# Kernel optimization log

Measured on AMD Instinct MI355X. Metric: run time of the kernel, lower is better.

Reference implementation:

```python
import jax, jax.numpy as jnp
import numpy as np

EMB = 1024
HEADS = 16
HEAD_DIM = EMB // HEADS
MASK_VAL = -10000.0


def setup_inputs() -> dict:
    key = jax.random.key(0)
    ks = jax.random.split(key, 5)
    B, S = 4, 2048
    x = jax.random.normal(ks[0], (B, S, EMB), dtype=jnp.float32)
    scale = 1.0 / np.sqrt(EMB)
    w_qkv = jax.random.normal(ks[1], (EMB, 3 * EMB), dtype=jnp.float32) * scale
    b_qkv = jnp.zeros((3 * EMB,), dtype=jnp.float32)
    w_fc = jax.random.normal(ks[2], (EMB, EMB), dtype=jnp.float32) * scale
    b_fc = jnp.zeros((EMB,), dtype=jnp.float32)
    return {"x": x, "w_qkv": w_qkv, "b_qkv": b_qkv, "w_fc": w_fc, "b_fc": b_fc}


def reference(x, w_qkv, b_qkv, w_fc, b_fc):
    B, S, _ = x.shape
    qkv = x @ w_qkv + b_qkv                      # (B, S, 3*EMB)
    q, k, v = jnp.split(qkv, 3, axis=-1)
    # split heads: (B, S, EMB) -> (B, H, S, Dh)
    def sh(t):
        return t.reshape(B, S, HEADS, HEAD_DIM).transpose(0, 2, 1, 3)
    q, k, v = sh(q), sh(k), sh(v)
    scores = jnp.einsum('bhqd,bhkd->bhqk', q, k) / np.sqrt(HEAD_DIM)
    causal = jnp.tril(jnp.ones((S, S), dtype=bool))[None, None]
    scores = jnp.where(causal, scores, jnp.float32(MASK_VAL))
    probs = jax.nn.softmax(scores, axis=-1)
    out = jnp.einsum('bhqk,bhkd->bhqd', probs, v)
    out = out.transpose(0, 2, 1, 3).reshape(B, S, EMB)  # merge heads
    return out @ w_fc + b_fc
```

## Files before the change

kernel.cpp:

```cpp
#include <hip/hip_runtime.h>
#include <hip/hip_bf16.h>
#include <cstdint>

#define BF16 __hip_bfloat16

typedef __attribute__((ext_vector_type(8))) short bhalf8;
typedef __attribute__((ext_vector_type(4))) float floatx4;

#define MFMA16(a, b, c) __builtin_amdgcn_mfma_f32_16x16x32_bf16((a), (b), (c), 0, 0, 0)

#define MASKV (-30000.0f)
#define QSCALE 0.18033688011112042f

__device__ __forceinline__ void async_cp16(const void* gsrc, void* ldst) {
  __builtin_amdgcn_global_load_lds(
      (__attribute__((address_space(1))) void*)(size_t)gsrc,
      (__attribute__((address_space(3))) void*)ldst, 16, 0, 0);
}

__device__ __forceinline__ bhalf8 cvt8(const float* p) {
  const float4 f0 = *(const float4*)p;
  const float4 f1 = *(const float4*)(p + 4);
  union { bhalf8 v; ushort u[8]; } r;
  const float t[8] = {f0.x, f0.y, f0.z, f0.w, f1.x, f1.y, f1.z, f1.w};
#pragma unroll
  for (int i = 0; i < 8; ++i) {
    BF16 h = __float2bfloat16(t[i]);
    r.u[i] = *(const ushort*)&h;
  }
  return r.v;
}

__global__ void cvt_f32_bf16(const float* __restrict__ in, BF16* __restrict__ out) {
  const size_t i = ((size_t)blockIdx.x * 256 + threadIdx.x) * 8;
  *(bhalf8*)(out + i) = cvt8(in + i);
}

__global__ void transpose_cvt(const float* __restrict__ in, ushort* __restrict__ out,
                              int R, int C) {
  __shared__ ushort t[32][33];
  const int c0 = blockIdx.x * 32, r0 = blockIdx.y * 32;
  const int tx = threadIdx.x, ty = threadIdx.y;
#pragma unroll
  for (int j = 0; j < 32; j += 8) {
    BF16 h = __float2bfloat16(in[(size_t)(r0 + ty + j) * C + c0 + tx]);
    t[ty + j][tx] = *(const ushort*)&h;
  }
  __syncthreads();
#pragma unroll
  for (int j = 0; j < 32; j += 8)
    out[(size_t)(c0 + ty + j) * R + r0 + tx] = t[tx][ty + j];
}

template <int MODE>
__global__ __launch_bounds__(256, 2) void gemm_bt(
    const BF16* __restrict__ A, const BF16* __restrict__ Bt, const float* __restrict__ bias,
    void* __restrict__ C0v, BF16* __restrict__ C1, BF16* __restrict__ C2,
    int Md, int Nd, int Kd) {
  __shared__ __align__(16) BF16 As[128 * 64];
  __shared__ __align__(16) BF16 Bs[128 * 64];

  const int tid = threadIdx.x;
  const int w = tid >> 6, lane = tid & 63;
  const int lm = lane & 15, quad = lane >> 4;
  const int wm = (w >> 1) * 64, wn = (w & 1) * 64;
  const int tile_m = blockIdx.y * 128, tile_n = blockIdx.x * 128;

  floatx4 acc[4][4];
#pragma unroll
  for (int i = 0; i < 4; ++i)
#pragma unroll
    for (int j = 0; j < 4; ++j) acc[i][j] = (floatx4){0.f, 0.f, 0.f, 0.f};

  for (int k0 = 0; k0 < Kd; k0 += 64) {
    __syncthreads();
#pragma unroll
    for (int j = 0; j < 4; ++j) {
      const int sb = (j * 4 + w) * 64;
      const int slot = sb + lane;
      const int row = slot >> 3;
      const int gs = ((slot & 7) - row) & 7;
      async_cp16(A + (size_t)(tile_m + row) * Kd + k0 + gs * 8, As + sb * 8);
      async_cp16(Bt + (size_t)(tile_n + row) * Kd + k0 + gs * 8, Bs + sb * 8);
    }
    __syncthreads();

#pragma unroll
    for (int s = 0; s < 2; ++s) {
      bhalf8 af[4], bfr[4];
#pragma unroll
      for (int mt = 0; mt < 4; ++mt) {
        const int r = wm + mt * 16 + lm;
        const int g = ((s * 4 + quad) + r) & 7;
        af[mt] = *(const bhalf8*)(As + r * 64 + g * 8);
      }
#pragma unroll
      for (int nt = 0; nt < 4; ++nt) {
        const int r = wn + nt * 16 + lm;
        const int g = ((s * 4 + quad) + r) & 7;
        bfr[nt] = *(const bhalf8*)(Bs + r * 64 + g * 8);
      }
#pragma unroll
      for (int mt = 0; mt < 4; ++mt)
#pragma unroll
        for (int nt = 0; nt < 4; ++nt)
          acc[mt][nt] = MFMA16(af[mt], bfr[nt], acc[mt][nt]);
    }
  }

#pragma unroll
  for (int nt = 0; nt < 4; ++nt) {
    const int n = tile_n + wn + nt * 16 + lm;
    const float bv = bias[n];
#pragma unroll
    for (int mt = 0; mt < 4; ++mt) {
      const int m0 = tile_m + wm + mt * 16 + quad * 4;
      floatx4 v = acc[mt][nt];
      if (MODE == 0) {
        float* C0f = (float*)C0v;
#pragma unroll
        for (int r = 0; r < 4; ++r)
          C0f[(size_t)(m0 + r) * Nd + n] = v[r] + bv;
      } else {
        const int which = n >> 10;
        const int h = (n >> 6) & 15;
        const int d = n & 63;
        if (which == 2) {
          const int b = m0 >> 11, s0 = m0 & 2047;
          union { ushort4 u4; ushort u[4]; } pk;
#pragma unroll
          for (int r = 0; r < 4; ++r) {
            BF16 hv = __float2bfloat16(v[r] + bv);
            pk.u[r] = *(const ushort*)&hv;
          }
          *(ushort4*)(C2 + ((size_t)((b * 16 + h) * 64 + d)) * 2048 + s0) = pk.u4;
        } else {
          BF16* dst = (which == 0) ? (BF16*)C0v : C1;
          const float sc = (which == 0) ? QSCALE : 1.0f;
#pragma unroll
          for (int r = 0; r < 4; ++r) {
            const int m = m0 + r, b = m >> 11, si = m & 2047;
            dst[((size_t)(b * 16 + h) * 2048 + si) * 64 + d] =
                __float2bfloat16((v[r] + bv) * sc);
          }
        }
      }
    }
  }
}

__global__ __launch_bounds__(256, 2) void flash_attn(
    const BF16* __restrict__ Q, const BF16* __restrict__ Kmat,
    const BF16* __restrict__ VT, BF16* __restrict__ O) {
  __shared__ __align__(16) BF16 Ks[64 * 64];
  __shared__ __align__(16) BF16 Vs[64 * 64];
  __shared__ __align__(16) BF16 Ps[4 * 32 * 64];

  const int bh = blockIdx.y;
  const int qt = (int)gridDim.x - 1 - (int)blockIdx.x;
  const int tid = threadIdx.x;
  const int w = tid >> 6, lane = tid & 63;
  const int lm = lane & 15, quad = lane >> 4;
  const size_t bh_off = (size_t)bh * (2048 * 64);

  const int qb0 = qt * 128 + w * 32;

  bhalf8 aq[2][2];
#pragma unroll
  for (int s2 = 0; s2 < 2; ++s2) {
    const size_t qoff = bh_off + (size_t)(qb0 + s2 * 16 + lm) * 64;
    aq[s2][0] = *(const bhalf8*)(Q + qoff + quad * 8);
    aq[s2][1] = *(const bhalf8*)(Q + qoff + 32 + quad * 8);
  }

  floatx4 oacc[2][4];
  float m_i[2], l_i[2];
#pragma unroll
  for (int s2 = 0; s2 < 2; ++s2) {
    m_i[s2] = MASKV;
    l_i[s2] = 0.f;
#pragma unroll
    for (int i = 0; i < 4; ++i) oacc[s2][i] = (floatx4){0.f, 0.f, 0.f, 0.f};
  }

  int srow[2], sgs[2], sslot[2];
#pragma unroll
  for (int j = 0; j < 2; ++j) {
    const int slot = (w * 2 + j) * 64 + lane;
    sslot[j] = slot;
    srow[j] = slot >> 3;
    sgs[j] = ((slot & 7) - (slot >> 3)) & 7;
  }
  BF16* pw = Ps + w * (32 * 64);

  bhalf8 kv[2], vv[2], nkv[2], nvv[2];
  {
    const BF16* Kg = Kmat + bh_off;
    const BF16* Vg = VT + bh_off;
#pragma unroll
    for (int j = 0; j < 2; ++j) {
      kv[j] = *(const bhalf8*)(Kg + srow[j] * 64 + sgs[j] * 8);
      vv[j] = *(const bhalf8*)(Vg + (size_t)srow[j] * 2048 + sgs[j] * 8);
    }
  }

  const int ktmax = 2 * qt + 1;
  for (int kt = 0; kt <= ktmax; ++kt) {
    __syncthreads();
#pragma unroll
    for (int j = 0; j < 2; ++j) {
      *(bhalf8*)(Ks + sslot[j] * 8) = kv[j];
      *(bhalf8*)(Vs + sslot[j] * 8) = vv[j];
    }
    __syncthreads();

    if (kt < ktmax) {
      const BF16* Kg = Kmat + bh_off + (size_t)((kt + 1) * 64) * 64;
      const BF16* Vg = VT + bh_off + (kt + 1) * 64;
#pragma unroll
      for (int j = 0; j < 2; ++j) {
        nkv[j] = *(const bhalf8*)(Kg + srow[j] * 64 + sgs[j] * 8);
        nvv[j] = *(const bhalf8*)(Vg + (size_t)srow[j] * 2048 + sgs[j] * 8);
      }
    }

    const int k0 = kt * 64;
#pragma unroll
    for (int s2 = 0; s2 < 2; ++s2) {
      const int qb = qb0 + s2 * 16;
      if (k0 > qb + 15) continue;

      floatx4 st[4];
#pragma unroll
      for (int nt = 0; nt < 4; ++nt) {
        const int rr = nt * 16 + lm;
        const bhalf8 ak0 = *(const bhalf8*)(Ks + rr * 64 + ((quad + rr) & 7) * 8);
        const bhalf8 ak1 = *(const bhalf8*)(Ks + rr * 64 + ((4 + quad + rr) & 7) * 8);
        floatx4 z = (floatx4){0.f, 0.f, 0.f, 0.f};
        z = MFMA16(ak0, aq[s2][0], z);
        z = MFMA16(ak1, aq[s2][1], z);
        st[nt] = z;
      }

      if (k0 + 63 > qb) {
#pragma unroll
        for (int nt = 0; nt < 4; ++nt)
#pragma unroll
          for (int r = 0; r < 4; ++r)
            if ((k0 + nt * 16 + quad * 4 + r) > (qb + lm)) st[nt][r] = MASKV;
      }

      float mx = MASKV;
#pragma unroll
      for (int nt = 0; nt < 4; ++nt)
#pragma unroll
        for (int r = 0; r < 4; ++r) mx = fmaxf(mx, st[nt][r]);
      mx = fmaxf(mx, __shfl_xor(mx, 16, 64));
      mx = fmaxf(mx, __shfl_xor(mx, 32, 64));
      const float mnew = fmaxf(m_i[s2], mx);
      const float alpha = __builtin_amdgcn_exp2f(m_i[s2] - mnew);
      m_i[s2] = mnew;

      float rs = 0.f;
#pragma unroll
      for (int nt = 0; nt < 4; ++nt)
#pragma unroll
        for (int r = 0; r < 4; ++r) {
          const float p = __builtin_amdgcn_exp2f(st[nt][r] - mnew);
          st[nt][r] = p;
          rs += p;
        }
      rs += __shfl_xor(rs, 16, 64);
      rs += __shfl_xor(rs, 32, 64);
      l_i[s2] = l_i[s2] * alpha + rs;
#pragma unroll
      for (int dn = 0; dn < 4; ++dn) oacc[s2][dn] *= alpha;

      BF16* pws = pw + s2 * (16 * 64);
#pragma unroll
      for (int nt = 0; nt < 4; ++nt) {
        union { ushort4 u4; ushort u[4]; } pk;
#pragma unroll
        for (int r = 0; r < 4; ++r) {
          BF16 h = __float2bfloat16(st[nt][r]);
          pk.u[r] = *(const ushort*)&h;
        }
        const int g = ((nt * 2 + (quad >> 1)) + lm) & 7;
        *(ushort4*)(pws + lm * 64 + g * 8 + (quad & 1) * 4) = pk.u4;
      }

      const bhalf8 ap0 = *(const bhalf8*)(pws + lm * 64 + ((quad + lm) & 7) * 8);
      const bhalf8 ap1 = *(const bhalf8*)(pws + lm * 64 + ((4 + quad + lm) & 7) * 8);
#pragma unroll
      for (int dn = 0; dn < 4; ++dn) {
        const int rr = dn * 16 + lm;
        const bhalf8 av0 = *(const bhalf8*)(Vs + rr * 64 + ((quad + rr) & 7) * 8);
        const bhalf8 av1 = *(const bhalf8*)(Vs + rr * 64 + ((4 + quad + rr) & 7) * 8);
        oacc[s2][dn] = MFMA16(av0, ap0, oacc[s2][dn]);
        oacc[s2][dn] = MFMA16(av1, ap1, oacc[s2][dn]);
      }
    }

#pragma unroll
    for (int j = 0; j < 2; ++j) { kv[j] = nkv[j]; vv[j] = nvv[j]; }
  }

  const int b = bh >> 4, h = bh & 15;
#pragma unroll
  for (int s2 = 0; s2 < 2; ++s2) {
    const float inv_l = 1.0f / l_i[s2];
    const size_t orow = (size_t)(b * 2048 + qb0 + s2 * 16 + lm) * 1024 + h * 64;
#pragma unroll
    for (int dn = 0; dn < 4; ++dn) {
      union { ushort4 u4; ushort u[4]; } pk;
#pragma unroll
      for (int r = 0; r < 4; ++r) {
        BF16 h2 = __float2bfloat16(oacc[s2][dn][r] * inv_l);
        pk.u[r] = *(const ushort*)&h2;
      }
      *(ushort4*)(O + orow + dn * 16 + quad * 4) = pk.u4;
    }
  }
}

extern "C" void kernel_launch(void* const* d_in, const int* in_sizes, int n_in,
                              void* d_out, int out_size, void* d_ws, size_t ws_size,
                              hipStream_t stream) {
  const float* x = (const float*)d_in[0];
  const float* w_qkv = (const float*)d_in[1];
  const float* b_qkv = (const float*)d_in[2];
  const float* w_fc = (const float*)d_in[3];
  const float* b_fc = (const float*)d_in[4];
  float* out = (float*)d_out;

  BF16* ws = (BF16*)d_ws;
  BF16* wTqkv = ws;
  BF16* wTfc = wTqkv + 3072 * 1024;
  BF16* xb = wTfc + 1024 * 1024;
  BF16* Qb = xb + 8388608;
  BF16* Kb = Qb + 8388608;
  BF16* VTb = Kb + 8388608;
  BF16* Ob = VTb + 8388608;

  cvt_f32_bf16<<<4096, 256, 0, stream>>>(x, xb);
  transpose_cvt<<<dim3(96, 32), dim3(32, 8), 0, stream>>>(w_qkv, (ushort*)wTqkv, 1024, 3072);
  transpose_cvt<<<dim3(32, 32), dim3(32, 8), 0, stream>>>(w_fc, (ushort*)wTfc, 1024, 1024);

  gemm_bt<1><<<dim3(24, 64), 256, 0, stream>>>(
      xb, wTqkv, b_qkv, (void*)Qb, Kb, VTb, 8192, 3072, 1024);
  flash_attn<<<dim3(16, 64), 256, 0, stream>>>(Qb, Kb, VTb, Ob);
  gemm_bt<0><<<dim3(8, 64), 256, 0, stream>>>(
      Ob, wTfc, b_fc, (void*)out, nullptr, nullptr, 8192, 1024, 1024);
}
```

Baseline: 309.3 us.

## Register-prefetch GEMM tiles and make flash attention per-wave with direct K/V loads

The GEMM drops global_load_lds async copies in favour of register double-buffering: the next K-slice is loaded into registers during the MFMAs and written to LDS at the top of the next iteration. Flash attention is restructured so each wave independently owns a 64-row query tile, and waves are paired as x, 15-x, 16+x and 31-x to balance causal work. K and V fragments are loaded straight from global memory into registers, which removes the shared K/V tiles and the block-wide barriers. The cost is more register pressure, since each wave now holds four query sub-tiles, and redundant global or L2 traffic because every wave fetches its own K/V.

After: 277.3 us. 1.12x faster.

```diff
diff --git a/kernel.cpp b/kernel.cpp
--- a/kernel.cpp
+++ b/kernel.cpp
@@ -11,12 +11,6 @@
 
 #define MASKV (-30000.0f)
 #define QSCALE 0.18033688011112042f
-
-__device__ __forceinline__ void async_cp16(const void* gsrc, void* ldst) {
-  __builtin_amdgcn_global_load_lds(
-      (__attribute__((address_space(1))) void*)(size_t)gsrc,
-      (__attribute__((address_space(3))) void*)ldst, 16, 0, 0);
-}
 
 __device__ __forceinline__ bhalf8 cvt8(const float* p) {
   const float4 f0 = *(const float4*)p;
@@ -72,18 +66,39 @@
 #pragma unroll
     for (int j = 0; j < 4; ++j) acc[i][j] = (floatx4){0.f, 0.f, 0.f, 0.f};
 
+  int srow[4], sgs[4], sslot[4];
+#pragma unroll
+  for (int j = 0; j < 4; ++j) {
+    const int slot = (j * 4 + w) * 64 + lane;
+    sslot[j] = slot;
+    srow[j] = slot >> 3;
+    sgs[j] = ((slot & 7) - (slot >> 3)) & 7;
+  }
+
+  bhalf8 va[4], vb[4], nva[4], nvb[4];
+#pragma unroll
+  for (int j = 0; j < 4; ++j) {
+    va[j] = *(const bhalf8*)(A + (size_t)(tile_m + srow[j]) * Kd + sgs[j] * 8);
+    vb[j] = *(const bhalf8*)(Bt + (size_t)(tile_n + srow[j]) * Kd + sgs[j] * 8);
+  }
+
   for (int k0 = 0; k0 < Kd; k0 += 64) {
     __syncthreads();
 #pragma unroll
     for (int j = 0; j < 4; ++j) {
-      const int sb = (j * 4 + w) * 64;
-      const int slot = sb + lane;
-      const int row = slot >> 3;
-      const int gs = ((slot & 7) - row) & 7;
-      async_cp16(A + (size_t)(tile_m + row) * Kd + k0 + gs * 8, As + sb * 8);
-      async_cp16(Bt + (size_t)(tile_n + row) * Kd + k0 + gs * 8, Bs + sb * 8);
+      *(bhalf8*)(As + sslot[j] * 8) = va[j];
+      *(bhalf8*)(Bs + sslot[j] * 8) = vb[j];
     }
     __syncthreads();
+
+    if (k0 + 64 < Kd) {
+      const int k1 = k0 + 64;
+#pragma unroll
+      for (int j = 0; j < 4; ++j) {
+        nva[j] = *(const bhalf8*)(A + (size_t)(tile_m + srow[j]) * Kd + k1 + sgs[j] * 8);
+        nvb[j] = *(const bhalf8*)(Bt + (size_t)(tile_n + srow[j]) * Kd + k1 + sgs[j] * 8);
+      }
+    }
 
 #pragma unroll
     for (int s = 0; s < 2; ++s) {
@@ -106,6 +121,8 @@
         for (int nt = 0; nt < 4; ++nt)
           acc[mt][nt] = MFMA16(af[mt], bfr[nt], acc[mt][nt]);
     }
+#pragma unroll
+    for (int j = 0; j < 4; ++j) { va[j] = nva[j]; vb[j] = nvb[j]; }
   }
 
 #pragma unroll
@@ -152,93 +169,60 @@
 __global__ __launch_bounds__(256, 2) void flash_attn(
     const BF16* __restrict__ Q, const BF16* __restrict__ Kmat,
     const BF16* __restrict__ VT, BF16* __restrict__ O) {
-  __shared__ __align__(16) BF16 Ks[64 * 64];
-  __shared__ __align__(16) BF16 Vs[64 * 64];
-  __shared__ __align__(16) BF16 Ps[4 * 32 * 64];
-
-  const int bh = blockIdx.y;
-  const int qt = (int)gridDim.x - 1 - (int)blockIdx.x;
+  __shared__ __align__(16) BF16 Ps[4][4][16 * 64];
+
   const int tid = threadIdx.x;
   const int w = tid >> 6, lane = tid & 63;
   const int lm = lane & 15, quad = lane >> 4;
+  const int bh = blockIdx.y;
+  const int x = blockIdx.x;
+  const int qt = (w == 0) ? x : (w == 1) ? (15 - x) : (w == 2) ? (16 + x) : (31 - x);
+  const int qb0 = qt * 64;
   const size_t bh_off = (size_t)bh * (2048 * 64);
 
-  const int qb0 = qt * 128 + w * 32;
-
-  bhalf8 aq[2][2];
-#pragma unroll
-  for (int s2 = 0; s2 < 2; ++s2) {
-    const size_t qoff = bh_off + (size_t)(qb0 + s2 * 16 + lm) * 64;
-    aq[s2][0] = *(const bhalf8*)(Q + qoff + quad * 8);
-    aq[s2][1] = *(const bhalf8*)(Q + qoff + 32 + quad * 8);
-  }
-
-  floatx4 oacc[2][4];
-  float m_i[2], l_i[2];
-#pragma unroll
-  for (int s2 = 0; s2 < 2; ++s2) {
+  bhalf8 aq[4][2];
+#pragma unroll
+  for (int s2 = 0; s2 < 4; ++s2) {
+    const BF16* qp = Q + bh_off + (size_t)(qb0 + s2 * 16 + lm) * 64 + quad * 8;
+    aq[s2][0] = *(const bhalf8*)qp;
+    aq[s2][1] = *(const bhalf8*)(qp + 32);
+  }
+
+  floatx4 oacc[4][4];
+  float m_i[4], l_i[4];
+#pragma unroll
+  for (int s2 = 0; s2 < 4; ++s2) {
     m_i[s2] = MASKV;
     l_i[s2] = 0.f;
 #pragma unroll
     for (int i = 0; i < 4; ++i) oacc[s2][i] = (floatx4){0.f, 0.f, 0.f, 0.f};
   }
 
-  int srow[2], sgs[2], sslot[2];
-#pragma unroll
-  for (int j = 0; j < 2; ++j) {
-    const int slot = (w * 2 + j) * 64 + lane;
-    sslot[j] = slot;
-    srow[j] = slot >> 3;
-    sgs[j] = ((slot & 7) - (slot >> 3)) & 7;
-  }
-  BF16* pw = Ps + w * (32 * 64);
-
-  bhalf8 kv[2], vv[2], nkv[2], nvv[2];
-  {
-    const BF16* Kg = Kmat + bh_off;
-    const BF16* Vg = VT + bh_off;
-#pragma unroll
-    for (int j = 0; j < 2; ++j) {
-      kv[j] = *(const bhalf8*)(Kg + srow[j] * 64 + sgs[j] * 8);
-      vv[j] = *(const bhalf8*)(Vg + (size_t)srow[j] * 2048 + sgs[j] * 8);
-    }
-  }
-
-  const int ktmax = 2 * qt + 1;
-  for (int kt = 0; kt <= ktmax; ++kt) {
-    __syncthreads();
-#pragma unroll
-    for (int j = 0; j < 2; ++j) {
-      *(bhalf8*)(Ks + sslot[j] * 8) = kv[j];
-      *(bhalf8*)(Vs + sslot[j] * 8) = vv[j];
-    }
-    __syncthreads();
-
-    if (kt < ktmax) {
-      const BF16* Kg = Kmat + bh_off + (size_t)((kt + 1) * 64) * 64;
-      const BF16* Vg = VT + bh_off + (kt + 1) * 64;
-#pragma unroll
-      for (int j = 0; j < 2; ++j) {
-        nkv[j] = *(const bhalf8*)(Kg + srow[j] * 64 + sgs[j] * 8);
-        nvv[j] = *(const bhalf8*)(Vg + (size_t)srow[j] * 2048 + sgs[j] * 8);
-      }
-    }
-
+  for (int kt = 0; kt <= qt; ++kt) {
     const int k0 = kt * 64;
-#pragma unroll
-    for (int s2 = 0; s2 < 2; ++s2) {
+
+    bhalf8 ak[4][2], av[4][2];
+#pragma unroll
+    for (int nt = 0; nt < 4; ++nt) {
+      const BF16* kp = Kmat + bh_off + (size_t)(k0 + nt * 16 + lm) * 64 + quad * 8;
+      ak[nt][0] = *(const bhalf8*)kp;
+      ak[nt][1] = *(const bhalf8*)(kp + 32);
+      const BF16* vp = VT + bh_off + (size_t)(nt * 16 + lm) * 2048 + k0 + quad * 8;
+      av[nt][0] = *(const bhalf8*)vp;
+      av[nt][1] = *(const bhalf8*)(vp + 32);
+    }
+
+#pragma unroll
+    for (int s2 = 0; s2 < 4; ++s2) {
       const int qb = qb0 + s2 * 16;
       if (k0 > qb + 15) continue;
 
       floatx4 st[4];
 #pragma unroll
       for (int nt = 0; nt < 4; ++nt) {
-        const int rr = nt * 16 + lm;
-        const bhalf8 ak0 = *(const bhalf8*)(Ks + rr * 64 + ((quad + rr) & 7) * 8);
-        const bhalf8 ak1 = *(const bhalf8*)(Ks + rr * 64 + ((4 + quad + rr) & 7) * 8);
         floatx4 z = (floatx4){0.f, 0.f, 0.f, 0.f};
-        z = MFMA16(ak0, aq[s2][0], z);
-        z = MFMA16(ak1, aq[s2][1], z);
+        z = MFMA16(ak[nt][0], aq[s2][0], z);
+        z = MFMA16(ak[nt][1], aq[s2][1], z);
         st[nt] = z;
       }
 
@@ -276,7 +260,7 @@
 #pragma unroll
       for (int dn = 0; dn < 4; ++dn) oacc[s2][dn] *= alpha;
 
-      BF16* pws = pw + s2 * (16 * 64);
+      BF16* pws = Ps[w][s2];
 #pragma unroll
       for (int nt = 0; nt < 4; ++nt) {
         union { ushort4 u4; ushort u[4]; } pk;
@@ -293,21 +277,15 @@
       const bhalf8 ap1 = *(const bhalf8*)(pws + lm * 64 + ((4 + quad + lm) & 7) * 8);
 #pragma unroll
       for (int dn = 0; dn < 4; ++dn) {
-        const int rr = dn * 16 + lm;
-        const bhalf8 av0 = *(const bhalf8*)(Vs + rr * 64 + ((quad + rr) & 7) * 8);
-        const bhalf8 av1 = *(const bhalf8*)(Vs + rr * 64 + ((4 + quad + rr) & 7) * 8);
-        oacc[s2][dn] = MFMA16(av0, ap0, oacc[s2][dn]);
-        oacc[s2][dn] = MFMA16(av1, ap1, oacc[s2][dn]);
-      }
-    }
-
-#pragma unroll
-    for (int j = 0; j < 2; ++j) { kv[j] = nkv[j]; vv[j] = nvv[j]; }
+        oacc[s2][dn] = MFMA16(av[dn][0], ap0, oacc[s2][dn]);
+        oacc[s2][dn] = MFMA16(av[dn][1], ap1, oacc[s2][dn]);
+      }
+    }
   }
 
   const int b = bh >> 4, h = bh & 15;
 #pragma unroll
-  for (int s2 = 0; s2 < 2; ++s2) {
+  for (int s2 = 0; s2 < 4; ++s2) {
     const float inv_l = 1.0f / l_i[s2];
     const size_t orow = (size_t)(b * 2048 + qb0 + s2 * 16 + lm) * 1024 + h * 64;
 #pragma unroll
@@ -348,7 +326,7 @@
 
   gemm_bt<1><<<dim3(24, 64), 256, 0, stream>>>(
       xb, wTqkv, b_qkv, (void*)Qb, Kb, VTb, 8192, 3072, 1024);
-  flash_attn<<<dim3(16, 64), 256, 0, stream>>>(Qb, Kb, VTb, Ob);
+  flash_attn<<<dim3(8, 64), 256, 0, stream>>>(Qb, Kb, VTb, Ob);
   gemm_bt<0><<<dim3(8, 64), 256, 0, stream>>>(
       Ob, wTfc, b_fc, (void*)out, nullptr, nullptr, 8192, 1024, 1024);
 }
```
